# Kernel optimization log

Measured on AMD Instinct MI355X. Metric: run time of the kernel, lower is better.

## Reference

```python
import jax, jax.numpy as jnp
import numpy as np

# ---- config (matches init_kwargs) ----
B, N, D = 16, 300, 256
HEADS, HD = 8, D // 8
FF = 1024
HID = FF // 2                      # SwiGLU hidden
SPATIAL = [(80, 80), (40, 40), (20, 20), (10, 10)]
LVL = len(SPATIAL)
NP = 4                              # points per level
TP = LVL * NP                       # total sampling points = 16
L = sum(h * w for h, w in SPATIAL)  # 8400
EPS = 1e-6


def setup_inputs() -> dict:
    key = jax.random.key(0)
    ks = jax.random.split(key, 24)
    s = 0.02
    return {
        "target": jax.random.normal(ks[0], (B, N, D), jnp.float32),
        "reference_points": jax.random.uniform(ks[1], (B, N, 1, 4), jnp.float32, 0.05, 0.95),
        "memory": jax.random.normal(ks[2], (B, L, D), jnp.float32),
        # self-attention
        "qkv_w": jax.random.normal(ks[3], (3 * D, D), jnp.float32) * s,
        "qkv_b": jnp.zeros((3 * D,), jnp.float32),
        "out_w": jax.random.normal(ks[4], (D, D), jnp.float32) * s,
        "out_b": jnp.zeros((D,), jnp.float32),
        "norm1_w": jnp.ones((D,), jnp.float32),
        # deformable cross-attention
        "off_w": jax.random.normal(ks[5], (HEADS * TP * 2, D), jnp.float32) * s,
        "off_b": jax.random.normal(ks[6], (HEADS * TP * 2,), jnp.float32) * 0.1,
        "aw_w": jax.random.normal(ks[7], (HEADS * TP, D), jnp.float32) * s,
        "aw_b": jnp.zeros((HEADS * TP,), jnp.float32),
        "cout_w": jax.random.normal(ks[8], (D, D), jnp.float32) * s,
        "cout_b": jnp.zeros((D,), jnp.float32),
        "norm2_w": jnp.ones((D,), jnp.float32),
        # SwiGLU FFN
        "w13": jax.random.normal(ks[9], (2 * HID, D), jnp.float32) * s,
        "w13_b": jnp.zeros((2 * HID,), jnp.float32),
        "w2": jax.random.normal(ks[10], (D, HID), jnp.float32) * s,
        "w2_b": jnp.zeros((D,), jnp.float32),
        "norm3_w": jnp.ones((D,), jnp.float32),
    }


def rmsnorm(x, w):
    return x * jax.lax.rsqrt(jnp.mean(x * x, axis=-1, keepdims=True) + EPS) * w


def bilinear_sample(vflat, loc, H, W):
    """vflat: (BH, hd, H*W); loc: (BH, Q, 2) in [0,1]. grid_sample align_corners=False, zero pad."""
    x = loc[..., 0] * W - 0.5
    y = loc[..., 1] * H - 0.5
    x0 = jnp.floor(x); y0 = jnp.floor(y)
    dx = x - x0; dy = y - y0
    x0i = x0.astype(jnp.int32); y0i = y0.astype(jnp.int32)

    def gather(xi, yi, w):
        valid = (xi >= 0) & (xi < W) & (yi >= 0) & (yi < H)
        idx = jnp.clip(yi, 0, H - 1) * W + jnp.clip(xi, 0, W - 1)
        g = jnp.take_along_axis(vflat, idx[:, None, :], axis=2)  # (BH, hd, Q)
        return g * (w * valid)[:, None, :]

    return (gather(x0i, y0i, (1 - dx) * (1 - dy))
            + gather(x0i + 1, y0i, dx * (1 - dy))
            + gather(x0i, y0i + 1, (1 - dx) * dy)
            + gather(x0i + 1, y0i + 1, dx * dy))


def reference(target, reference_points, memory, qkv_w, qkv_b, out_w, out_b, norm1_w,
              off_w, off_b, aw_w, aw_b, cout_w, cout_b, norm2_w,
              w13, w13_b, w2, w2_b, norm3_w):
    # ---------- self-attention (query_pos_embed=None, attn_mask=None) ----------
    qkv = target @ qkv_w.T + qkv_b                    # (B,N,3D)
    qkv = qkv.reshape(B, N, 3, HEADS, HD).transpose(2, 0, 3, 1, 4)
    q, k, v = qkv[0], qkv[1], qkv[2]                  # (B,H,N,hd)
    attn = jax.nn.softmax(jnp.einsum("bhqd,bhkd->bhqk", q, k) / np.sqrt(HD), axis=-1)
    sa = jnp.einsum("bhqk,bhkd->bhqd", attn, v).transpose(0, 2, 1, 3).reshape(B, N, D)
    x = rmsnorm(target + (sa @ out_w.T + out_b), norm1_w)

    # ---------- deformable cross-attention ----------
    # value_op: memory -> per-head value (B,H,hd,L)
    val = memory.reshape(B, L, HEADS, HD).transpose(0, 2, 3, 1).reshape(B * HEADS, HD, L)

    offsets = (x @ off_w.T + off_b).reshape(B, N, HEADS, TP, 2)
    aw = jax.nn.softmax((x @ aw_w.T + aw_b).reshape(B, N, HEADS, TP), axis=-1)

    ref_xy = reference_points[:, :, :, None, :2]      # (B,N,1,1,2)
    ref_wh = reference_points[:, :, :, None, 2:]
    pts_scale = 1.0 / NP
    loc = ref_xy + offsets * pts_scale * ref_wh * 0.5  # (B,N,H,TP,2)
    loc = loc.transpose(0, 2, 1, 3, 4).reshape(B * HEADS, N, TP, 2)

    sampled = []
    start = 0
    for li, (H, W) in enumerate(SPATIAL):
        v_l = jax.lax.dynamic_slice_in_dim(val, start, H * W, axis=2)
        loc_l = loc[:, :, li * NP:(li + 1) * NP, :].reshape(B * HEADS, N * NP, 2)
        s = bilinear_sample(v_l, loc_l, H, W).reshape(B * HEADS, HD, N, NP)
        sampled.append(s)
        start += H * W
    sampled = jnp.concatenate(sampled, axis=-1)        # (BH, hd, N, TP)

    w = aw.transpose(0, 2, 1, 3).reshape(B * HEADS, 1, N, TP)
    ca = (sampled * w).sum(-1)                         # (BH, hd, N)
    ca = ca.reshape(B, HEADS, HD, N).transpose(0, 3, 1, 2).reshape(B, N, D)
    ca = ca @ cout_w.T + cout_b

    x = rmsnorm(x + ca, norm2_w)

    # ---------- SwiGLU FFN ----------
    h = x @ w13.T + w13_b
    h1, h2 = h[..., :HID], h[..., HID:]
    ffn = (jax.nn.silu(h1) * h2) @ w2.T + w2_b
    x = jnp.clip(x + ffn, -65504.0, 65504.0)
    return rmsnorm(x, norm3_w)
```

## Files before the change

### kernel.cpp

```cpp
#include <hip/hip_runtime.h>
#include <cstdint>
#include <cstddef>


typedef __attribute__((ext_vector_type(8))) short bf16x8;
typedef __attribute__((ext_vector_type(4))) float f32x4;

__device__ __forceinline__ unsigned short f2bf(float f) {
  unsigned int u = __float_as_uint(f);
  u = (u + 0x7fffu + ((u >> 16) & 1u)) >> 16;
  return (unsigned short)u;
}
__device__ __forceinline__ unsigned int pack2bf(float lo, float hi) {
  return ((unsigned int)f2bf(hi) << 16) | (unsigned int)f2bf(lo);
}

__device__ __forceinline__ void gemm_dev(
    const float* __restrict__ A, const float* __restrict__ W,
    const float* __restrict__ bias, float* __restrict__ C,
    int N, int K, int row0, int col0,
    unsigned short* As, unsigned short* Ws)
{
  const int t = threadIdx.x, wave = t >> 6, lane = t & 63;
  const int lr = lane & 15, g = lane >> 4;
  const int sr = t >> 4, sc = (t & 15) * 4;

  float4 ra[4], rw[8];
  const float* Ab = A + (size_t)(row0 + sr) * K + sc;
  const float* Wb = W + (size_t)(col0 + sr) * K + sc;

#pragma unroll
  for (int i = 0; i < 4; ++i) ra[i] = *(const float4*)(Ab + (size_t)16 * i * K);
#pragma unroll
  for (int j = 0; j < 8; ++j) rw[j] = *(const float4*)(Wb + (size_t)16 * j * K);

  f32x4 acc[4][2] = {};

  for (int k0 = 0; k0 < K; k0 += 64) {
    __syncthreads();
#pragma unroll
    for (int i = 0; i < 4; ++i) {
      uint2 p;
      p.x = pack2bf(ra[i].x, ra[i].y);
      p.y = pack2bf(ra[i].z, ra[i].w);
      *(uint2*)&As[(sr + 16 * i) * 72 + sc] = p;
    }
#pragma unroll
    for (int j = 0; j < 8; ++j) {
      uint2 p;
      p.x = pack2bf(rw[j].x, rw[j].y);
      p.y = pack2bf(rw[j].z, rw[j].w);
      *(uint2*)&Ws[(sr + 16 * j) * 72 + sc] = p;
    }
    __syncthreads();

    if (k0 + 64 < K) {
#pragma unroll
      for (int i = 0; i < 4; ++i)
        ra[i] = *(const float4*)(Ab + (size_t)16 * i * K + k0 + 64);
#pragma unroll
      for (int j = 0; j < 8; ++j)
        rw[j] = *(const float4*)(Wb + (size_t)16 * j * K + k0 + 64);
    }

#pragma unroll
    for (int ks = 0; ks < 2; ++ks) {
      bf16x8 aA[4], bB[2];
#pragma unroll
      for (int i = 0; i < 4; ++i)
        aA[i] = *(const bf16x8*)&As[(i * 16 + lr) * 72 + ks * 32 + g * 8];
#pragma unroll
      for (int j = 0; j < 2; ++j)
        bB[j] = *(const bf16x8*)&Ws[(wave * 32 + j * 16 + lr) * 72 + ks * 32 + g * 8];
#pragma unroll
      for (int i = 0; i < 4; ++i)
#pragma unroll
        for (int j = 0; j < 2; ++j)
          acc[i][j] = __builtin_amdgcn_mfma_f32_16x16x32_bf16(aA[i], bB[j], acc[i][j], 0, 0, 0);
    }
  }

  const float b0 = bias[col0 + wave * 32 + lr];
  const float b1 = bias[col0 + wave * 32 + 16 + lr];
#pragma unroll
  for (int i = 0; i < 4; ++i) {
#pragma unroll
    for (int r = 0; r < 4; ++r) {
      const int row = row0 + i * 16 + g * 4 + r;
      float* dst = &C[(size_t)row * N + col0 + wave * 32 + lr];
      dst[0]  = acc[i][0][r] + b0;
      dst[16] = acc[i][1][r] + b1;
    }
  }
}

__global__ __launch_bounds__(256) void gemm_mfma(
    const float* __restrict__ A, const float* __restrict__ W,
    const float* __restrict__ bias, float* __restrict__ C, int N, int K)
{
  __shared__ __align__(16) unsigned short As[64 * 72];
  __shared__ __align__(16) unsigned short Ws[128 * 72];
  gemm_dev(A, W, bias, C, N, K, blockIdx.y * 64, blockIdx.x * 128, As, Ws);
}

__global__ __launch_bounds__(256) void gemm_offaw(
    const float* __restrict__ X,
    const float* __restrict__ off_w, const float* __restrict__ off_b, float* __restrict__ OF,
    const float* __restrict__ aw_w, const float* __restrict__ aw_b, float* __restrict__ AW,
    int K)
{
  __shared__ __align__(16) unsigned short As[64 * 72];
  __shared__ __align__(16) unsigned short Ws[128 * 72];
  if (blockIdx.x < 2)
    gemm_dev(X, off_w, off_b, OF, 256, K, blockIdx.y * 64, blockIdx.x * 128, As, Ws);
  else
    gemm_dev(X, aw_w, aw_b, AW, 128, K, blockIdx.y * 64, 0, As, Ws);
}

template <bool SWIGLU>
__global__ __launch_bounds__(256) void gemm_rms32(
    const float* __restrict__ A, const float* __restrict__ W,
    const float* __restrict__ bias, const float* __restrict__ res,
    const float* __restrict__ nw, float* __restrict__ C,
    int K, int clip)
{
  __shared__ __align__(16) unsigned short As[32 * 72];
  __shared__ __align__(16) unsigned short Ws[256 * 72];
  __shared__ float rsum[32][4];

  const int t = threadIdx.x, wave = t >> 6, lane = t & 63;
  const int lr = lane & 15, g = lane >> 4;
  const int row0 = blockIdx.x * 32;
  const int sr = t >> 4, sc = (t & 15) * 4;
  const int Astride = SWIGLU ? 1024 : K;

  float4 ra1[2], ra2[2], rw[16];
  const float* Ab = A + (size_t)(row0 + sr) * Astride + sc;
  const float* Wb = W + (size_t)sr * K + sc;

#pragma unroll
  for (int i = 0; i < 2; ++i) {
    ra1[i] = *(const float4*)(Ab + (size_t)16 * i * Astride);
    if (SWIGLU) ra2[i] = *(const float4*)(Ab + (size_t)16 * i * Astride + 512);
  }
#pragma unroll
  for (int j = 0; j < 16; ++j) rw[j] = *(const float4*)(Wb + (size_t)16 * j * K);

  f32x4 acc[2][4] = {};

  for (int k0 = 0; k0 < K; k0 += 64) {
    __syncthreads();
#pragma unroll
    for (int i = 0; i < 2; ++i) {
      float4 v;
      if (SWIGLU) {
        v.x = ra1[i].x / (1.f + __expf(-ra1[i].x)) * ra2[i].x;
        v.y = ra1[i].y / (1.f + __expf(-ra1[i].y)) * ra2[i].y;
        v.z = ra1[i].z / (1.f + __expf(-ra1[i].z)) * ra2[i].z;
        v.w = ra1[i].w / (1.f + __expf(-ra1[i].w)) * ra2[i].w;
      } else {
        v = ra1[i];
      }
      uint2 p;
      p.x = pack2bf(v.x, v.y);
      p.y = pack2bf(v.z, v.w);
      *(uint2*)&As[(sr + 16 * i) * 72 + sc] = p;
    }
#pragma unroll
    for (int j = 0; j < 16; ++j) {
      uint2 p;
      p.x = pack2bf(rw[j].x, rw[j].y);
      p.y = pack2bf(rw[j].z, rw[j].w);
      *(uint2*)&Ws[(sr + 16 * j) * 72 + sc] = p;
    }
    __syncthreads();

    if (k0 + 64 < K) {
#pragma unroll
      for (int i = 0; i < 2; ++i) {
        ra1[i] = *(const float4*)(Ab + (size_t)16 * i * Astride + k0 + 64);
        if (SWIGLU) ra2[i] = *(const float4*)(Ab + (size_t)16 * i * Astride + 512 + k0 + 64);
      }
#pragma unroll
      for (int j = 0; j < 16; ++j)
        rw[j] = *(const float4*)(Wb + (size_t)16 * j * K + k0 + 64);
    }

#pragma unroll
    for (int ks = 0; ks < 2; ++ks) {
      bf16x8 aA[2], bB[4];
#pragma unroll
      for (int i = 0; i < 2; ++i)
        aA[i] = *(const bf16x8*)&As[(i * 16 + lr) * 72 + ks * 32 + g * 8];
#pragma unroll
      for (int j = 0; j < 4; ++j)
        bB[j] = *(const bf16x8*)&Ws[(wave * 64 + j * 16 + lr) * 72 + ks * 32 + g * 8];
#pragma unroll
      for (int i = 0; i < 2; ++i)
#pragma unroll
        for (int j = 0; j < 4; ++j)
          acc[i][j] = __builtin_amdgcn_mfma_f32_16x16x32_bf16(aA[i], bB[j], acc[i][j], 0, 0, 0);
    }
  }

  float bj[4], wj[4];
#pragma unroll
  for (int j = 0; j < 4; ++j) {
    bj[j] = bias[wave * 64 + j * 16 + lr];
    wj[j] = nw[wave * 64 + j * 16 + lr];
  }

  float part[2][4] = {};
#pragma unroll
  for (int i = 0; i < 2; ++i) {
#pragma unroll
    for (int r = 0; r < 4; ++r) {
      const int row = row0 + i * 16 + g * 4 + r;
#pragma unroll
      for (int j = 0; j < 4; ++j) {
        const int col = wave * 64 + j * 16 + lr;
        float v = acc[i][j][r] + bj[j] + res[(size_t)row * 256 + col];
        if (clip) v = fminf(fmaxf(v, -65504.f), 65504.f);
        acc[i][j][r] = v;
        part[i][r] += v * v;
      }
    }
  }
#pragma unroll
  for (int i = 0; i < 2; ++i)
#pragma unroll
    for (int r = 0; r < 4; ++r) {
      float s = part[i][r];
      s += __shfl_xor(s, 1);
      s += __shfl_xor(s, 2);
      s += __shfl_xor(s, 4);
      s += __shfl_xor(s, 8);
      part[i][r] = s;
    }
  if (lr == 0) {
#pragma unroll
    for (int i = 0; i < 2; ++i)
#pragma unroll
      for (int r = 0; r < 4; ++r)
        rsum[i * 16 + g * 4 + r][wave] = part[i][r];
  }
  __syncthreads();

#pragma unroll
  for (int i = 0; i < 2; ++i) {
#pragma unroll
    for (int r = 0; r < 4; ++r) {
      const int row = row0 + i * 16 + g * 4 + r;
      const f32x4 q = *(const f32x4*)&rsum[i * 16 + g * 4 + r][0];
      const float tot = q[0] + q[1] + q[2] + q[3];
      const float scale = rsqrtf(tot * (1.0f / 256.0f) + 1e-6f);
#pragma unroll
      for (int j = 0; j < 4; ++j) {
        const int col = wave * 64 + j * 16 + lr;
        C[(size_t)row * 256 + col] = acc[i][j][r] * scale * wj[j];
      }
    }
  }
}

__global__ __launch_bounds__(256) void gemm_qkv(
    const float* __restrict__ A, const float* __restrict__ W,
    const float* __restrict__ bias,
    unsigned short* __restrict__ Qb, unsigned short* __restrict__ Kb,
    unsigned short* __restrict__ VTb)
{
  __shared__ __align__(16) unsigned short As[64 * 72];
  __shared__ __align__(16) unsigned short Ws[128 * 72];
  const int K = 256;
  const int t = threadIdx.x, wave = t >> 6, lane = t & 63;
  const int lr = lane & 15, g = lane >> 4;
  const int row0 = blockIdx.y * 64, col0 = blockIdx.x * 128;
  const int sr = t >> 4, sc = (t & 15) * 4;

  float4 ra[4], rw[8];
  const float* Ab = A + (size_t)(row0 + sr) * K + sc;
  const float* Wb = W + (size_t)(col0 + sr) * K + sc;

#pragma unroll
  for (int i = 0; i < 4; ++i) ra[i] = *(const float4*)(Ab + (size_t)16 * i * K);
#pragma unroll
  for (int j = 0; j < 8; ++j) rw[j] = *(const float4*)(Wb + (size_t)16 * j * K);

  f32x4 acc[4][2] = {};

  for (int k0 = 0; k0 < K; k0 += 64) {
    __syncthreads();
#pragma unroll
    for (int i = 0; i < 4; ++i) {
      uint2 p;
      p.x = pack2bf(ra[i].x, ra[i].y);
      p.y = pack2bf(ra[i].z, ra[i].w);
      *(uint2*)&As[(sr + 16 * i) * 72 + sc] = p;
    }
#pragma unroll
    for (int j = 0; j < 8; ++j) {
      uint2 p;
      p.x = pack2bf(rw[j].x, rw[j].y);
      p.y = pack2bf(rw[j].z, rw[j].w);
      *(uint2*)&Ws[(sr + 16 * j) * 72 + sc] = p;
    }
    __syncthreads();

    if (k0 + 64 < K) {
#pragma unroll
      for (int i = 0; i < 4; ++i)
        ra[i] = *(const float4*)(Ab + (size_t)16 * i * K + k0 + 64);
#pragma unroll
      for (int j = 0; j < 8; ++j)
        rw[j] = *(const float4*)(Wb + (size_t)16 * j * K + k0 + 64);
    }

#pragma unroll
    for (int ks = 0; ks < 2; ++ks) {
      bf16x8 aA[4], bB[2];
#pragma unroll
      for (int i = 0; i < 4; ++i)
        aA[i] = *(const bf16x8*)&As[(i * 16 + lr) * 72 + ks * 32 + g * 8];
#pragma unroll
      for (int j = 0; j < 2; ++j)
        bB[j] = *(const bf16x8*)&Ws[(wave * 32 + j * 16 + lr) * 72 + ks * 32 + g * 8];
#pragma unroll
      for (int i = 0; i < 4; ++i)
#pragma unroll
        for (int j = 0; j < 2; ++j)
          acc[i][j] = __builtin_amdgcn_mfma_f32_16x16x32_bf16(aA[i], bB[j], acc[i][j], 0, 0, 0);
    }
  }

  const int bx = blockIdx.x;
  const float scale = 0.17677669529663687f;
  const float b0 = bias[col0 + wave * 32 + lr];
  const float b1 = bias[col0 + wave * 32 + 16 + lr];

  if (bx < 4) {
    unsigned short* dstT = (bx < 2) ? Qb : Kb;
    const float mul = (bx < 2) ? scale : 1.0f;
#pragma unroll
    for (int i = 0; i < 4; ++i) {
#pragma unroll
      for (int r = 0; r < 4; ++r) {
        const int row = row0 + i * 16 + g * 4 + r;
        const int b = row / 300, n = row - b * 300;
#pragma unroll
        for (int j = 0; j < 2; ++j) {
          const int c768 = col0 + wave * 32 + j * 16 + lr;
          const int h = (c768 >> 5) & 7, c = c768 & 31;
          const float v = (acc[i][j][r] + (j ? b1 : b0)) * mul;
          dstT[((size_t)(b * 8 + h) * 304 + n) * 32 + c] = f2bf(v);
        }
      }
    }
  } else {
    __syncthreads();
#pragma unroll
    for (int i = 0; i < 4; ++i)
#pragma unroll
      for (int r = 0; r < 4; ++r)
#pragma unroll
        for (int j = 0; j < 2; ++j) {
          const int c_local = wave * 32 + j * 16 + lr;
          const int n_local = i * 16 + g * 4 + r;
          Ws[c_local * 72 + n_local] = f2bf(acc[i][j][r] + (j ? b1 : b0));
        }
    __syncthreads();
    for (int idx = t; idx < 128 * 64; idx += 256) {
      const int c_local = idx >> 6, n_local = idx & 63;
      const int row = row0 + n_local;
      const int b = row / 300, n = row - b * 300;
      const int c768 = col0 + c_local;
      const int h = (c768 >> 5) & 7, c = c768 & 31;
      VTb[((size_t)(b * 8 + h) * 32 + c) * 320 + n] = Ws[c_local * 72 + n_local];
    }
    if (blockIdx.y == 74) {
      for (int idx = t; idx < 64 * 32 * 20; idx += 256) {
        const int n = 300 + idx % 20;
        const int rem = idx / 20;
        const int c = rem & 31, bh4 = rem >> 5;
        const int b = bh4 >> 2, h = (bx - 4) * 4 + (bh4 & 3);
        VTb[((size_t)(b * 8 + h) * 32 + c) * 320 + n] = 0;
      }
    }
  }
}

__global__ __launch_bounds__(64) void attn_core(
    const unsigned short* __restrict__ Qb, const unsigned short* __restrict__ Kb,
    const unsigned short* __restrict__ VTb, float* __restrict__ sa)
{
  __shared__ __align__(16) unsigned short P[16 * 40];
  const int gt = blockIdx.x;
  const int bh = blockIdx.y, b = bh >> 3, h = bh & 7;
  const int lane = threadIdx.x, lr = lane & 15, g = lane >> 4;

  const unsigned short* Kbase = Kb + (size_t)bh * 304 * 32;
  const unsigned short* Vbase = VTb + (size_t)bh * 32 * 320;

  bf16x8 aQ = *(const bf16x8*)&Qb[((size_t)bh * 304 + gt * 16 + lr) * 32 + g * 8];

  f32x4 s[19];
  const f32x4 zero = {0.f, 0.f, 0.f, 0.f};
#pragma unroll
  for (int kt = 0; kt < 19; ++kt) {
    bf16x8 bK = *(const bf16x8*)&Kbase[(kt * 16 + lr) * 32 + g * 8];
    s[kt] = __builtin_amdgcn_mfma_f32_16x16x32_bf16(aQ, bK, zero, 0, 0, 0);
  }
  if (lr >= 12) {
    s[18][0] = -1e30f; s[18][1] = -1e30f; s[18][2] = -1e30f; s[18][3] = -1e30f;
  }

  float inv[4];
#pragma unroll
  for (int r = 0; r < 4; ++r) {
    float m = -1e30f;
#pragma unroll
    for (int kt = 0; kt < 19; ++kt) m = fmaxf(m, s[kt][r]);
#pragma unroll
    for (int o = 8; o >= 1; o >>= 1) m = fmaxf(m, __shfl_xor(m, o));
    float sum = 0.f;
#pragma unroll
    for (int kt = 0; kt < 19; ++kt) {
      float e = __expf(s[kt][r] - m);
      s[kt][r] = e;
      sum += e;
    }
#pragma unroll
    for (int o = 8; o >= 1; o >>= 1) sum += __shfl_xor(sum, o);
    inv[r] = 1.f / sum;
  }

  f32x4 o0 = {0.f, 0.f, 0.f, 0.f}, o1 = {0.f, 0.f, 0.f, 0.f};
#pragma unroll
  for (int ks = 0; ks < 10; ++ks) {
#pragma unroll
    for (int tp = 0; tp < 2; ++tp) {
      const int kt = ks * 2 + tp;
#pragma unroll
      for (int r = 0; r < 4; ++r) {
        unsigned short pv = (kt < 19) ? f2bf(s[kt][r]) : (unsigned short)0;
        P[(g * 4 + r) * 40 + tp * 16 + lr] = pv;
      }
    }
    asm volatile("s_waitcnt lgkmcnt(0)" ::: "memory");
    __builtin_amdgcn_sched_barrier(0);
    bf16x8 aP = *(const bf16x8*)&P[lr * 40 + g * 8];
    bf16x8 bV0 = *(const bf16x8*)&Vbase[(size_t)lr * 320 + ks * 32 + g * 8];
    bf16x8 bV1 = *(const bf16x8*)&Vbase[(size_t)(16 + lr) * 320 + ks * 32 + g * 8];
    o0 = __builtin_amdgcn_mfma_f32_16x16x32_bf16(aP, bV0, o0, 0, 0, 0);
    o1 = __builtin_amdgcn_mfma_f32_16x16x32_bf16(aP, bV1, o1, 0, 0, 0);
  }

#pragma unroll
  for (int r = 0; r < 4; ++r) {
    const int q = gt * 16 + g * 4 + r;
    if (q < 300) {
      const float iv = inv[r];
      float* dst = &sa[((size_t)b * 300 + q) * 256 + h * 32];
      dst[lr] = o0[r] * iv;
      dst[16 + lr] = o1[r] * iv;
    }
  }
}

__global__ __launch_bounds__(256) void deform_k(
    const float* __restrict__ memory, const float* __restrict__ refp,
    const float* __restrict__ OFF, const float* __restrict__ AW,
    float* __restrict__ ca)
{
  __shared__ float locx[8][16], locy[8][16], wgt[8][16];
  const int bn = blockIdx.x, b = bn / 300, t = threadIdx.x;

  if (t < 128) {
    int h = t >> 4, p = t & 15;
    float cx = refp[(size_t)bn * 4 + 0], cy = refp[(size_t)bn * 4 + 1];
    float rw = refp[(size_t)bn * 4 + 2], rh = refp[(size_t)bn * 4 + 3];
    float ox = OFF[(size_t)bn * 256 + h * 32 + p * 2 + 0];
    float oy = OFF[(size_t)bn * 256 + h * 32 + p * 2 + 1];
    locx[h][p] = cx + ox * 0.125f * rw;
    locy[h][p] = cy + oy * 0.125f * rh;
    float av = AW[(size_t)bn * 128 + t];
    float mx = av;
#pragma unroll
    for (int o = 8; o; o >>= 1) mx = fmaxf(mx, __shfl_xor(mx, o));
    float e = __expf(av - mx);
    float ssum = e;
#pragma unroll
    for (int o = 8; o; o >>= 1) ssum += __shfl_xor(ssum, o);
    wgt[h][p] = e / ssum;
  }
  __syncthreads();

  const int h = t >> 5, hd = t & 31;
  const float* mb = memory + (size_t)b * 8500 * 256 + h * 32 + hd;
  float acc = 0.f;
#pragma unroll
  for (int p = 0; p < 16; ++p) {
    const int HWs[4] = {80, 40, 20, 10};
    const int Sts[4] = {0, 6400, 8000, 8400};
    const int li = p >> 2;
    const int Hh = HWs[li], Ww = HWs[li], st = Sts[li];
    float x = locx[h][p] * (float)Ww - 0.5f;
    float y = locy[h][p] * (float)Hh - 0.5f;
    float x0f = floorf(x), y0f = floorf(y);
    float dx = x - x0f, dy = y - y0f;
    int x0 = (int)x0f, y0 = (int)y0f;
    float awp = wgt[h][p];
#pragma unroll
    for (int cc = 0; cc < 4; ++cc) {
      int xi = x0 + (cc & 1), yi = y0 + (cc >> 1);
      float wc = ((cc & 1) ? dx : 1.f - dx) * ((cc >> 1) ? dy : 1.f - dy);
      bool valid = (xi >= 0) && (xi < Ww) && (yi >= 0) && (yi < Hh);
      int xc = xi < 0 ? 0 : (xi >= Ww ? Ww - 1 : xi);
      int yc = yi < 0 ? 0 : (yi >= Hh ? Hh - 1 : yi);
      float gv = mb[(size_t)(st + yc * Ww + xc) * 256];
      acc += gv * (valid ? wc * awp : 0.f);
    }
  }
  ca[(size_t)bn * 256 + t] = acc;
}

extern "C" void kernel_launch(void* const* d_in, const int* in_sizes, int n_in,
                              void* d_out, int out_size, void* d_ws, size_t ws_size,
                              hipStream_t stream)
{
  (void)in_sizes; (void)n_in; (void)out_size; (void)ws_size;
  const float* target  = (const float*)d_in[0];
  const float* refp    = (const float*)d_in[1];
  const float* memory  = (const float*)d_in[2];
  const float* qkv_w   = (const float*)d_in[3];
  const float* qkv_b   = (const float*)d_in[4];
  const float* out_w   = (const float*)d_in[5];
  const float* out_b   = (const float*)d_in[6];
  const float* norm1_w = (const float*)d_in[7];
  const float* off_w   = (const float*)d_in[8];
  const float* off_b   = (const float*)d_in[9];
  const float* aw_w    = (const float*)d_in[10];
  const float* aw_b    = (const float*)d_in[11];
  const float* cout_w  = (const float*)d_in[12];
  const float* cout_b  = (const float*)d_in[13];
  const float* norm2_w = (const float*)d_in[14];
  const float* w13     = (const float*)d_in[15];
  const float* w13_b   = (const float*)d_in[16];
  const float* w2      = (const float*)d_in[17];
  const float* w2_b    = (const float*)d_in[18];
  const float* norm3_w = (const float*)d_in[19];
  float* out = (float*)d_out;

  float* ws  = (float*)d_ws;
  float* SA  = ws;
  float* X   = SA  + 4800 * 256;
  float* OF  = X   + 4800 * 256;
  float* AWb = OF  + 4800 * 256;
  float* CA  = AWb + 4800 * 128;
  float* X2  = CA  + 4800 * 256;
  float* Hb  = X2  + 4800 * 256;
  unsigned short* Qb  = (unsigned short*)(Hb + 4800 * 1024);
  unsigned short* Kb  = Qb + 128 * 304 * 32;
  unsigned short* VTb = Kb + 128 * 304 * 32;

  dim3 blk(256);

  gemm_qkv<<<dim3(6, 75), blk, 0, stream>>>(target, qkv_w, qkv_b, Qb, Kb, VTb);
  attn_core<<<dim3(19, 128), dim3(64), 0, stream>>>(Qb, Kb, VTb, SA);
  gemm_rms32<false><<<150, blk, 0, stream>>>(SA, out_w, out_b, target, norm1_w, X, 256, 0);
  gemm_offaw<<<dim3(3, 75), blk, 0, stream>>>(X, off_w, off_b, OF, aw_w, aw_b, AWb, 256);
  deform_k<<<4800, blk, 0, stream>>>(memory, refp, OF, AWb, CA);
  gemm_rms32<false><<<150, blk, 0, stream>>>(CA, cout_w, cout_b, X, norm2_w, X2, 256, 0);
  gemm_mfma<<<dim3(8, 75), blk, 0, stream>>>(X2, w13, w13_b, Hb, 1024, 256);
  gemm_rms32<true><<<150, blk, 0, stream>>>(Hb, w2, w2_b, X2, norm3_w, out, 512, 1);
}
```

Measured before the change: 131.0 us.

## Fuse out-projection, offset/weight GEMM and deformable sampling into one kernel

Replaces three kernels with a single 150-block kernel. Each block takes 32 query rows and does three things in turn: the output projection with residual and RMSNorm, then the offset and attention-weight GEMM, then the softmax and bilinear deformable gather. The OF and AW intermediates stay in LDS and never reach global memory, and the normalized activations are reused from LDS as bf16. Block IDs are also remapped across XCDs. The cost is that the gather phase, which before ran as 4800 blocks, now runs 32 rows sequentially per block over only 150 blocks, which sharply cuts the parallelism available to hide memory latency.

```diff
diff --git a/kernel.cpp b/kernel.cpp
--- a/kernel.cpp
+++ b/kernel.cpp
@@ -101,20 +101,6 @@
   __shared__ __align__(16) unsigned short As[64 * 72];
   __shared__ __align__(16) unsigned short Ws[128 * 72];
   gemm_dev(A, W, bias, C, N, K, blockIdx.y * 64, blockIdx.x * 128, As, Ws);
-}
-
-__global__ __launch_bounds__(256) void gemm_offaw(
-    const float* __restrict__ X,
-    const float* __restrict__ off_w, const float* __restrict__ off_b, float* __restrict__ OF,
-    const float* __restrict__ aw_w, const float* __restrict__ aw_b, float* __restrict__ AW,
-    int K)
-{
-  __shared__ __align__(16) unsigned short As[64 * 72];
-  __shared__ __align__(16) unsigned short Ws[128 * 72];
-  if (blockIdx.x < 2)
-    gemm_dev(X, off_w, off_b, OF, 256, K, blockIdx.y * 64, blockIdx.x * 128, As, Ws);
-  else
-    gemm_dev(X, aw_w, aw_b, AW, 128, K, blockIdx.y * 64, 0, As, Ws);
 }
 
 template <bool SWIGLU>
@@ -259,6 +245,275 @@
         const int col = wave * 64 + j * 16 + lr;
         C[(size_t)row * 256 + col] = acc[i][j][r] * scale * wj[j];
       }
+    }
+  }
+}
+
+__global__ __launch_bounds__(256) void fused_mid(
+    const float* __restrict__ SA, const float* __restrict__ out_w,
+    const float* __restrict__ out_b, const float* __restrict__ target,
+    const float* __restrict__ norm1_w, float* __restrict__ X,
+    const float* __restrict__ off_w, const float* __restrict__ off_b,
+    const float* __restrict__ aw_w, const float* __restrict__ aw_b,
+    const float* __restrict__ refp, const float* __restrict__ memory,
+    float* __restrict__ CA)
+{
+  __shared__ __align__(16) unsigned short As[32 * 72];
+  __shared__ __align__(16) unsigned short Wsu[384 * 72];
+  __shared__ __align__(16) unsigned short X16[4][32 * 72];
+  __shared__ float rsum[32][4];
+
+  const int t = threadIdx.x, wave = t >> 6, lane = t & 63;
+  const int lr = lane & 15, g = lane >> 4;
+  const int bi = blockIdx.x, xcd = bi & 7, pos = bi >> 3;
+  const int wgid = (xcd < 6 ? xcd * 19 : 114 + (xcd - 6) * 18) + pos;
+  const int row0 = wgid * 32;
+  const int sr = t >> 4, sc = (t & 15) * 4;
+
+  {
+    const int K = 256;
+    float4 ra1[2], rw[16];
+    const float* Ab = SA + (size_t)(row0 + sr) * K + sc;
+    const float* Wb = out_w + (size_t)sr * K + sc;
+
+#pragma unroll
+    for (int i = 0; i < 2; ++i) ra1[i] = *(const float4*)(Ab + (size_t)16 * i * K);
+#pragma unroll
+    for (int j = 0; j < 16; ++j) rw[j] = *(const float4*)(Wb + (size_t)16 * j * K);
+
+    f32x4 acc[2][4] = {};
+
+    for (int k0 = 0; k0 < K; k0 += 64) {
+      __syncthreads();
+#pragma unroll
+      for (int i = 0; i < 2; ++i) {
+        uint2 p;
+        p.x = pack2bf(ra1[i].x, ra1[i].y);
+        p.y = pack2bf(ra1[i].z, ra1[i].w);
+        *(uint2*)&As[(sr + 16 * i) * 72 + sc] = p;
+      }
+#pragma unroll
+      for (int j = 0; j < 16; ++j) {
+        uint2 p;
+        p.x = pack2bf(rw[j].x, rw[j].y);
+        p.y = pack2bf(rw[j].z, rw[j].w);
+        *(uint2*)&Wsu[(sr + 16 * j) * 72 + sc] = p;
+      }
+      __syncthreads();
+
+      if (k0 + 64 < K) {
+#pragma unroll
+        for (int i = 0; i < 2; ++i)
+          ra1[i] = *(const float4*)(Ab + (size_t)16 * i * K + k0 + 64);
+#pragma unroll
+        for (int j = 0; j < 16; ++j)
+          rw[j] = *(const float4*)(Wb + (size_t)16 * j * K + k0 + 64);
+      }
+
+#pragma unroll
+      for (int ks = 0; ks < 2; ++ks) {
+        bf16x8 aA[2], bB[4];
+#pragma unroll
+        for (int i = 0; i < 2; ++i)
+          aA[i] = *(const bf16x8*)&As[(i * 16 + lr) * 72 + ks * 32 + g * 8];
+#pragma unroll
+        for (int j = 0; j < 4; ++j)
+          bB[j] = *(const bf16x8*)&Wsu[(wave * 64 + j * 16 + lr) * 72 + ks * 32 + g * 8];
+#pragma unroll
+        for (int i = 0; i < 2; ++i)
+#pragma unroll
+          for (int j = 0; j < 4; ++j)
+            acc[i][j] = __builtin_amdgcn_mfma_f32_16x16x32_bf16(aA[i], bB[j], acc[i][j], 0, 0, 0);
+      }
+    }
+
+    float bj[4], wj[4];
+#pragma unroll
+    for (int j = 0; j < 4; ++j) {
+      bj[j] = out_b[wave * 64 + j * 16 + lr];
+      wj[j] = norm1_w[wave * 64 + j * 16 + lr];
+    }
+
+    float part[2][4] = {};
+#pragma unroll
+    for (int i = 0; i < 2; ++i) {
+#pragma unroll
+      for (int r = 0; r < 4; ++r) {
+        const int row = row0 + i * 16 + g * 4 + r;
+#pragma unroll
+        for (int j = 0; j < 4; ++j) {
+          const int col = wave * 64 + j * 16 + lr;
+          float v = acc[i][j][r] + bj[j] + target[(size_t)row * 256 + col];
+          acc[i][j][r] = v;
+          part[i][r] += v * v;
+        }
+      }
+    }
+#pragma unroll
+    for (int i = 0; i < 2; ++i)
+#pragma unroll
+      for (int r = 0; r < 4; ++r) {
+        float s = part[i][r];
+        s += __shfl_xor(s, 1);
+        s += __shfl_xor(s, 2);
+        s += __shfl_xor(s, 4);
+        s += __shfl_xor(s, 8);
+        part[i][r] = s;
+      }
+    if (lr == 0) {
+#pragma unroll
+      for (int i = 0; i < 2; ++i)
+#pragma unroll
+        for (int r = 0; r < 4; ++r)
+          rsum[i * 16 + g * 4 + r][wave] = part[i][r];
+    }
+    __syncthreads();
+
+#pragma unroll
+    for (int i = 0; i < 2; ++i) {
+#pragma unroll
+      for (int r = 0; r < 4; ++r) {
+        const int row_l = i * 16 + g * 4 + r;
+        const int row = row0 + row_l;
+        const f32x4 q = *(const f32x4*)&rsum[row_l][0];
+        const float tot = q[0] + q[1] + q[2] + q[3];
+        const float scale = rsqrtf(tot * (1.0f / 256.0f) + 1e-6f);
+#pragma unroll
+        for (int j = 0; j < 4; ++j) {
+          const int col = wave * 64 + j * 16 + lr;
+          const float o = acc[i][j][r] * scale * wj[j];
+          X[(size_t)row * 256 + col] = o;
+          X16[wave][row_l * 72 + j * 16 + lr] = f2bf(o);
+        }
+      }
+    }
+  }
+  __syncthreads();
+
+  float* OFa = (float*)Wsu;
+  float* AWa = OFa + 32 * 258;
+  {
+    f32x4 acc2[2][6] = {};
+    for (int k0 = 0; k0 < 256; k0 += 64) {
+#pragma unroll
+      for (int s = 0; s < 24; ++s) {
+        const int slot = t + s * 256;
+        const int row = slot >> 4, fc = (slot & 15) * 4;
+        const float* wp = (row < 256) ? (off_w + (size_t)row * 256)
+                                      : (aw_w + (size_t)(row - 256) * 256);
+        const float4 v = *(const float4*)(wp + k0 + fc);
+        uint2 p;
+        p.x = pack2bf(v.x, v.y);
+        p.y = pack2bf(v.z, v.w);
+        *(uint2*)&Wsu[row * 72 + fc] = p;
+      }
+      __syncthreads();
+
+#pragma unroll
+      for (int ks = 0; ks < 2; ++ks) {
+        bf16x8 aA[2], bB[6];
+#pragma unroll
+        for (int i = 0; i < 2; ++i)
+          aA[i] = *(const bf16x8*)&X16[k0 >> 6][(i * 16 + lr) * 72 + ks * 32 + g * 8];
+#pragma unroll
+        for (int j = 0; j < 6; ++j)
+          bB[j] = *(const bf16x8*)&Wsu[(wave * 96 + j * 16 + lr) * 72 + ks * 32 + g * 8];
+#pragma unroll
+        for (int i = 0; i < 2; ++i)
+#pragma unroll
+          for (int j = 0; j < 6; ++j)
+            acc2[i][j] = __builtin_amdgcn_mfma_f32_16x16x32_bf16(aA[i], bB[j], acc2[i][j], 0, 0, 0);
+      }
+      __syncthreads();
+    }
+
+    float bj2[6];
+#pragma unroll
+    for (int j = 0; j < 6; ++j) {
+      const int col = wave * 96 + j * 16 + lr;
+      bj2[j] = (col < 256) ? off_b[col] : aw_b[col - 256];
+    }
+#pragma unroll
+    for (int i = 0; i < 2; ++i)
+#pragma unroll
+      for (int r = 0; r < 4; ++r) {
+        const int row_l = i * 16 + g * 4 + r;
+#pragma unroll
+        for (int j = 0; j < 6; ++j) {
+          const int col = wave * 96 + j * 16 + lr;
+          const float v = acc2[i][j][r] + bj2[j];
+          if (col < 256) OFa[row_l * 258 + col] = v;
+          else           AWa[row_l * 130 + (col - 256)] = v;
+        }
+      }
+  }
+  __syncthreads();
+
+  float* locx = (float*)Wsu;
+  float* locy = locx + 4096;
+  float* wgt  = locx + 8192;
+  {
+    const int r = t >> 3, h = t & 7;
+    const int bn = row0 + r;
+    const float cx = refp[(size_t)bn * 4 + 0], cy = refp[(size_t)bn * 4 + 1];
+    const float rw_ = refp[(size_t)bn * 4 + 2], rh = refp[(size_t)bn * 4 + 3];
+    float lx[16], ly[16], wp[16];
+    float mx = -1e30f;
+#pragma unroll
+    for (int p = 0; p < 16; ++p) {
+      lx[p] = cx + OFa[r * 258 + h * 32 + p * 2]     * 0.125f * rw_;
+      ly[p] = cy + OFa[r * 258 + h * 32 + p * 2 + 1] * 0.125f * rh;
+      wp[p] = AWa[r * 130 + h * 16 + p];
+      mx = fmaxf(mx, wp[p]);
+    }
+    float ssum = 0.f;
+#pragma unroll
+    for (int p = 0; p < 16; ++p) {
+      wp[p] = __expf(wp[p] - mx);
+      ssum += wp[p];
+    }
+    const float inv = 1.f / ssum;
+    __syncthreads();
+#pragma unroll
+    for (int p = 0; p < 16; ++p) {
+      locx[r * 128 + h * 16 + p] = lx[p];
+      locy[r * 128 + h * 16 + p] = ly[p];
+      wgt [r * 128 + h * 16 + p] = wp[p] * inv;
+    }
+  }
+  __syncthreads();
+
+  {
+    const int h = t >> 5, hd = t & 31;
+    for (int r = 0; r < 32; ++r) {
+      const int bn = row0 + r;
+      const int b = bn / 300;
+      const float* mb = memory + (size_t)b * 8500 * 256 + h * 32 + hd;
+      float acc = 0.f;
+#pragma unroll
+      for (int p = 0; p < 16; ++p) {
+        const int HWs[4] = {80, 40, 20, 10};
+        const int Sts[4] = {0, 6400, 8000, 8400};
+        const int li = p >> 2;
+        const int Hh = HWs[li], Ww = HWs[li], st = Sts[li];
+        const float x = locx[r * 128 + h * 16 + p] * (float)Ww - 0.5f;
+        const float y = locy[r * 128 + h * 16 + p] * (float)Hh - 0.5f;
+        const float x0f = floorf(x), y0f = floorf(y);
+        const float dx = x - x0f, dy = y - y0f;
+        const int x0 = (int)x0f, y0 = (int)y0f;
+        const float awp = wgt[r * 128 + h * 16 + p];
+#pragma unroll
+        for (int cc = 0; cc < 4; ++cc) {
+          const int xi = x0 + (cc & 1), yi = y0 + (cc >> 1);
+          const float wc = ((cc & 1) ? dx : 1.f - dx) * ((cc >> 1) ? dy : 1.f - dy);
+          const bool valid = (xi >= 0) && (xi < Ww) && (yi >= 0) && (yi < Hh);
+          const int xc = xi < 0 ? 0 : (xi >= Ww ? Ww - 1 : xi);
+          const int yc = yi < 0 ? 0 : (yi >= Hh ? Hh - 1 : yi);
+          const float gv = mb[(size_t)(st + yc * Ww + xc) * 256];
+          acc += gv * (valid ? wc * awp : 0.f);
+        }
+      }
+      CA[(size_t)bn * 256 + t] = acc;
     }
   }
 }
@@ -464,63 +719,6 @@
       dst[16 + lr] = o1[r] * iv;
     }
   }
-}
-
-__global__ __launch_bounds__(256) void deform_k(
-    const float* __restrict__ memory, const float* __restrict__ refp,
-    const float* __restrict__ OFF, const float* __restrict__ AW,
-    float* __restrict__ ca)
-{
-  __shared__ float locx[8][16], locy[8][16], wgt[8][16];
-  const int bn = blockIdx.x, b = bn / 300, t = threadIdx.x;
-
-  if (t < 128) {
-    int h = t >> 4, p = t & 15;
-    float cx = refp[(size_t)bn * 4 + 0], cy = refp[(size_t)bn * 4 + 1];
-    float rw = refp[(size_t)bn * 4 + 2], rh = refp[(size_t)bn * 4 + 3];
-    float ox = OFF[(size_t)bn * 256 + h * 32 + p * 2 + 0];
-    float oy = OFF[(size_t)bn * 256 + h * 32 + p * 2 + 1];
-    locx[h][p] = cx + ox * 0.125f * rw;
-    locy[h][p] = cy + oy * 0.125f * rh;
-    float av = AW[(size_t)bn * 128 + t];
-    float mx = av;
-#pragma unroll
-    for (int o = 8; o; o >>= 1) mx = fmaxf(mx, __shfl_xor(mx, o));
-    float e = __expf(av - mx);
-    float ssum = e;
-#pragma unroll
-    for (int o = 8; o; o >>= 1) ssum += __shfl_xor(ssum, o);
-    wgt[h][p] = e / ssum;
-  }
-  __syncthreads();
-
-  const int h = t >> 5, hd = t & 31;
-  const float* mb = memory + (size_t)b * 8500 * 256 + h * 32 + hd;
-  float acc = 0.f;
-#pragma unroll
-  for (int p = 0; p < 16; ++p) {
-    const int HWs[4] = {80, 40, 20, 10};
-    const int Sts[4] = {0, 6400, 8000, 8400};
-    const int li = p >> 2;
-    const int Hh = HWs[li], Ww = HWs[li], st = Sts[li];
-    float x = locx[h][p] * (float)Ww - 0.5f;
-    float y = locy[h][p] * (float)Hh - 0.5f;
-    float x0f = floorf(x), y0f = floorf(y);
-    float dx = x - x0f, dy = y - y0f;
-    int x0 = (int)x0f, y0 = (int)y0f;
-    float awp = wgt[h][p];
-#pragma unroll
-    for (int cc = 0; cc < 4; ++cc) {
-      int xi = x0 + (cc & 1), yi = y0 + (cc >> 1);
-      float wc = ((cc & 1) ? dx : 1.f - dx) * ((cc >> 1) ? dy : 1.f - dy);
-      bool valid = (xi >= 0) && (xi < Ww) && (yi >= 0) && (yi < Hh);
-      int xc = xi < 0 ? 0 : (xi >= Ww ? Ww - 1 : xi);
-      int yc = yi < 0 ? 0 : (yi >= Hh ? Hh - 1 : yi);
-      float gv = mb[(size_t)(st + yc * Ww + xc) * 256];
-      acc += gv * (valid ? wc * awp : 0.f);
-    }
-  }
-  ca[(size_t)bn * 256 + t] = acc;
 }
 
 extern "C" void kernel_launch(void* const* d_in, const int* in_sizes, int n_in,
@@ -553,9 +751,7 @@
   float* ws  = (float*)d_ws;
   float* SA  = ws;
   float* X   = SA  + 4800 * 256;
-  float* OF  = X   + 4800 * 256;
-  float* AWb = OF  + 4800 * 256;
-  float* CA  = AWb + 4800 * 128;
+  float* CA  = X   + 4800 * 256;
   float* X2  = CA  + 4800 * 256;
   float* Hb  = X2  + 4800 * 256;
   unsigned short* Qb  = (unsigned short*)(Hb + 4800 * 1024);
@@ -566,9 +762,8 @@
 
   gemm_qkv<<<dim3(6, 75), blk, 0, stream>>>(target, qkv_w, qkv_b, Qb, Kb, VTb);
   attn_core<<<dim3(19, 128), dim3(64), 0, stream>>>(Qb, Kb, VTb, SA);
-  gemm_rms32<false><<<150, blk, 0, stream>>>(SA, out_w, out_b, target, norm1_w, X, 256, 0);
-  gemm_offaw<<<dim3(3, 75), blk, 0, stream>>>(X, off_w, off_b, OF, aw_w, aw_b, AWb, 256);
-  deform_k<<<4800, blk, 0, stream>>>(memory, refp, OF, AWb, CA);
+  fused_mid<<<150, blk, 0, stream>>>(SA, out_w, out_b, target, norm1_w, X,
+                                     off_w, off_b, aw_w, aw_b, refp, memory, CA);
   gemm_rms32<false><<<150, blk, 0, stream>>>(CA, cout_w, cout_b, X, norm2_w, X2, 256, 0);
   gemm_mfma<<<dim3(8, 75), blk, 0, stream>>>(X2, w13, w13_b, Hb, 1024, 256);
   gemm_rms32<true><<<150, blk, 0, stream>>>(Hb, w2, w2_b, X2, norm3_w, out, 512, 1);
```

Result: slower. 421.2 us (+221.5%).
